# Kernel optimization log

Hardware: AMD Instinct MI355X
Metric: run time of the kernel (lower is better)

## Reference

```python
import jax, jax.numpy as jnp
import numpy as np

B, S, H, NH = 1, 4096, 1024, 16
DH = H // NH


def setup_inputs() -> dict:
    key = jax.random.key(0)
    ks = jax.random.split(key, 9)
    sc = 0.02
    return {
        "queries": jax.random.normal(ks[0], (B, S, H), jnp.float32),
        "keys": jax.random.normal(ks[1], (B, S, H), jnp.float32),
        "values": jax.random.normal(ks[2], (B, S, H), jnp.float32),
        "Wq_w": jax.random.normal(ks[3], (H, H), jnp.float32) * sc,
        "Wq_b": jax.random.normal(ks[4], (H,), jnp.float32) * sc,
        "Wk_w": jax.random.normal(ks[5], (H, H), jnp.float32) * sc,
        "Wk_b": jax.random.normal(ks[6], (H,), jnp.float32) * sc,
        "Wv_w": jax.random.normal(ks[7], (H, H), jnp.float32) * sc,
        "Wv_b": jax.random.normal(ks[8], (H,), jnp.float32) * sc,
    }


def _split_heads(x):
    # torch.chunk(x, NH, dim=-1) then stack(dim=1) == reshape + transpose
    b, s, h = x.shape
    return jnp.transpose(x.reshape(b, s, NH, DH), (0, 2, 1, 3))  # [B,NH,S,DH]


def reference(queries, keys, values, Wq_w, Wq_b, Wk_w, Wk_b, Wv_w, Wv_b):
    q = jax.nn.relu(queries @ Wq_w.T + Wq_b)
    k = jax.nn.relu(keys @ Wk_w.T + Wk_b)
    v = jax.nn.relu(values @ Wv_w.T + Wv_b)
    qh, kh, vh = _split_heads(q), _split_heads(k), _split_heads(v)
    score = jnp.einsum("bhsd,bhtd->bhst", qh, kh) / jnp.sqrt(jnp.float32(DH))
    attn = jax.nn.softmax(score, axis=-1)
    a = jnp.einsum("bhst,bhtd->bhsd", attn, vh)  # [B,NH,S,DH]
    # faithful to torch: permute(0,1,3,2) -> [B,NH,DH,S], then reshape to (B,S,H)
    a = jnp.transpose(a, (0, 1, 3, 2)).reshape(q.shape[0], q.shape[1], q.shape[2])
    return a + queries
```

## Files before the change

kernel.cpp:

```cpp
#include <hip/hip_runtime.h>
#include <stdint.h>


#define SEQ 4096
#define HID 1024
#define NHEAD 16
#define DHEAD 64

typedef __attribute__((ext_vector_type(8))) short short8_t;
typedef __attribute__((ext_vector_type(4))) float f32x4;
typedef __attribute__((ext_vector_type(16))) float f32x16;
typedef __attribute__((ext_vector_type(2))) unsigned int u32x2;

#define WS_QB   0u
#define WS_KB   4194304u
#define WS_VB   8388608u
#define WS_WQ   12582912u
#define WS_QO   15728640u
#define WS_KO   19922944u
#define WS_VT   24117248u

__device__ __forceinline__ unsigned short f2bf(float f) {
  union { float f; unsigned int u; } x; x.f = f;
  unsigned int u = x.u;
  return (unsigned short)((u + 0x7FFFu + ((u >> 16) & 1u)) >> 16);
}

__device__ __forceinline__ float fexp2(float x) {
#if __has_builtin(__builtin_amdgcn_exp2f)
  return __builtin_amdgcn_exp2f(x);
#else
  float r; asm("v_exp_f32 %0, %1" : "=v"(r) : "v"(x)); return r;
#endif
}

__device__ __forceinline__ unsigned int pk2(float a, float b) {
  unsigned int r;
  asm("v_cvt_pk_bf16_f32 %0, %1, %2" : "=v"(r) : "v"(a), "v"(b));
  return r;
}

__device__ __forceinline__ void pl32swap(unsigned int& a, unsigned int& b) {
  asm("v_permlane32_swap_b32 %0, %1" : "+v"(a), "+v"(b));
}

__device__ __forceinline__ void gll16(const void* g, void* l) {
  __builtin_amdgcn_global_load_lds(
      (const __attribute__((address_space(1))) void*)g,
      (__attribute__((address_space(3))) void*)l, 16, 0, 0);
}

__device__ __forceinline__ void packP(const f32x16& a, short8_t& p0,
                                      short8_t& p1) {
  unsigned int w0 = pk2(a[0], a[1]),   w1 = pk2(a[2], a[3]);
  unsigned int w2 = pk2(a[4], a[5]),   w3 = pk2(a[6], a[7]);
  unsigned int w4 = pk2(a[8], a[9]),   w5 = pk2(a[10], a[11]);
  unsigned int w6 = pk2(a[12], a[13]), w7 = pk2(a[14], a[15]);
  pl32swap(w0, w2);
  pl32swap(w1, w3);
  pl32swap(w4, w6);
  pl32swap(w5, w7);
  union { unsigned int u[4]; short8_t v; } q0, q1;
  q0.u[0] = w0; q0.u[1] = w1; q0.u[2] = w2; q0.u[3] = w3;
  q1.u[0] = w4; q1.u[1] = w5; q1.u[2] = w6; q1.u[3] = w7;
  p0 = q0.v; p1 = q1.v;
}

#define MFMA32(a, b, c) __builtin_amdgcn_mfma_f32_32x32x16_bf16(a, b, c, 0, 0, 0)

__global__ void __launch_bounds__(256) prep_convert(
    const float* __restrict__ qin, const float* __restrict__ kin,
    const float* __restrict__ vin, const float* __restrict__ wq,
    const float* __restrict__ wk, const float* __restrict__ wv,
    unsigned short* __restrict__ ws) {
  const int total = 3932160;
  for (int i = blockIdx.x * blockDim.x + threadIdx.x; i < total;
       i += gridDim.x * blockDim.x) {
    const float* src; unsigned short* dst; int off;
    if (i < 3145728) {
      int which = i >> 20;
      off = (i & 1048575) << 2;
      src = which == 0 ? qin : (which == 1 ? kin : vin);
      dst = ws + which * 4194304u;
    } else {
      int j = i - 3145728;
      int which = j >> 18;
      off = (j & 262143) << 2;
      src = which == 0 ? wq : (which == 1 ? wk : wv);
      dst = ws + WS_WQ + which * 1048576u;
    }
    float4 f = *(const float4*)(src + off);
    u32x2 p;
    p.x = f2bf(f.x) | ((unsigned int)f2bf(f.y) << 16);
    p.y = f2bf(f.z) | ((unsigned int)f2bf(f.w) << 16);
    *(u32x2*)(dst + off) = p;
  }
}

__global__ void __launch_bounds__(256) qkv_gemm(
    unsigned short* __restrict__ ws, const float* __restrict__ bq,
    const float* __restrict__ bk, const float* __restrict__ bv) {
  __shared__ alignas(16) unsigned short lA[128 * 64];
  __shared__ alignas(16) unsigned short lB[128 * 64];
  const int z = blockIdx.z;
  const unsigned short* A = ws + z * 4194304u;
  const unsigned short* W = ws + WS_WQ + z * 1048576u;
  const float* bias = z == 0 ? bq : (z == 1 ? bk : bv);
  const int tid = threadIdx.x;
  const int lane = tid & 63;
  const int wid = tid >> 6;
  const int wr = wid >> 1, wc = wid & 1;
  const int lin = blockIdx.y * 8 + blockIdx.x;
  const int nid = (lin & 7) * 32 + (lin >> 3);
  const int bm = nid >> 3, bn = nid & 7;
  const int l15 = lane & 15, l4 = lane >> 4;

  f32x4 acc[4][4];
#pragma unroll
  for (int m = 0; m < 4; ++m)
#pragma unroll
    for (int n = 0; n < 4; ++n) acc[m][n] = {0.f, 0.f, 0.f, 0.f};

  const int srow = tid >> 3;
  const int sch = tid & 7;

  for (int kt = 0; kt < 1024; kt += 64) {
    __syncthreads();
#pragma unroll
    for (int r = 0; r < 4; ++r) {
      const int row = r * 32 + srow;
      const int ch = sch ^ (row & 7);
      gll16(A + (size_t)(bm * 128 + row) * 1024 + kt + ch * 8,
            (char*)lA + r * 4096 + wid * 1024);
      gll16(W + (size_t)(bn * 128 + row) * 1024 + kt + ch * 8,
            (char*)lB + r * 4096 + wid * 1024);
    }
    __syncthreads();
    short8_t af[4][2], bf[4][2];
#pragma unroll
    for (int m = 0; m < 4; ++m) {
      const int row = wr * 64 + m * 16 + l15;
#pragma unroll
      for (int kk = 0; kk < 2; ++kk)
        af[m][kk] = *(const short8_t*)(
            (const char*)lA + row * 128 + (((kk * 4 + l4) ^ (row & 7)) * 16));
    }
#pragma unroll
    for (int n = 0; n < 4; ++n) {
      const int row = wc * 64 + n * 16 + l15;
#pragma unroll
      for (int kk = 0; kk < 2; ++kk)
        bf[n][kk] = *(const short8_t*)(
            (const char*)lB + row * 128 + (((kk * 4 + l4) ^ (row & 7)) * 16));
    }
#pragma unroll
    for (int m = 0; m < 4; ++m)
#pragma unroll
      for (int n = 0; n < 4; ++n)
#pragma unroll
        for (int kk = 0; kk < 2; ++kk)
          acc[m][n] = __builtin_amdgcn_mfma_f32_16x16x32_bf16(
              af[m][kk], bf[n][kk], acc[m][n], 0, 0, 0);
  }

  const int row0 = bm * 128 + wr * 64;
  const int col0 = bn * 128 + wc * 64;
  if (z < 2) {
    const float scl = (z == 1) ? 0.18033688011112042f : 1.0f;
    unsigned short* o = ws + WS_QO + z * 4194304u;
#pragma unroll
    for (int n = 0; n < 4; ++n) {
      const int col = col0 + n * 16 + l15;
      const float bb = bias[col];
#pragma unroll
      for (int m = 0; m < 4; ++m)
#pragma unroll
        for (int j = 0; j < 4; ++j) {
          const int row = row0 + m * 16 + l4 * 4 + j;
          o[(size_t)row * 1024 + col] = f2bf(fmaxf(acc[m][n][j] + bb, 0.f) * scl);
        }
    }
  } else {
    unsigned short* vt = ws + WS_VT;
#pragma unroll
    for (int n = 0; n < 4; ++n) {
      const int col = col0 + n * 16 + l15;
      const float bb = bias[col];
      const int nh = col >> 6, d = col & 63;
#pragma unroll
      for (int m = 0; m < 4; ++m) {
        const int t0 = row0 + m * 16 + l4 * 4;
        u32x2 p;
        p.x = f2bf(fmaxf(acc[m][n][0] + bb, 0.f)) |
              ((unsigned int)f2bf(fmaxf(acc[m][n][1] + bb, 0.f)) << 16);
        p.y = f2bf(fmaxf(acc[m][n][2] + bb, 0.f)) |
              ((unsigned int)f2bf(fmaxf(acc[m][n][3] + bb, 0.f)) << 16);
        *(u32x2*)(vt + (size_t)nh * 262144 + (size_t)d * 4096 + t0) = p;
      }
    }
  }
}

__global__ void __launch_bounds__(512, 4) attn_fwd(
    const unsigned short* __restrict__ ws, const float* __restrict__ qin,
    float* __restrict__ out) {
  __shared__ alignas(16) char smem[32768];
  const char* lKb = smem;
  const char* lVb = smem + 16384;
  float* fO = (float*)smem;
  float* fRs = (float*)(smem + 16896);

  const unsigned short* qo = ws + WS_QO;
  const char* koB = (const char*)(ws + WS_KO);
  const char* vtB = (const char*)(ws + WS_VT);
  const int nh = blockIdx.y;
  const int qb0 = blockIdx.x * 128;
  const int tid = threadIdx.x, lane = tid & 63, wid = tid >> 6;
  const int l31 = lane & 31, l5 = lane >> 5;
  const int qg = wid >> 1, tw = wid & 1;
  const int sq = qb0 + qg * 32 + l31;

  const int stt = tid >> 3;
  const int sch = tid & 7;
  const unsigned kgoff =
      (unsigned)(stt * 1024 + nh * 64 + ((sch ^ (stt & 7)) * 8)) * 2u;
  const unsigned vgoff =
      (unsigned)(nh * 262144 + stt * 4096 + ((sch ^ (stt & 7)) * 8)) * 2u;
  const unsigned ldst = (unsigned)tid * 16u;

  short8_t qf[4];
#pragma unroll
  for (int kcd = 0; kcd < 4; ++kcd)
    qf[kcd] = *(const short8_t*)(qo + (size_t)sq * 1024 + nh * 64 +
                                 kcd * 16 + l5 * 8);

  int kofl[4];
  {
    const int row = tw * 32 + l31;
#pragma unroll
    for (int kcd = 0; kcd < 4; ++kcd)
      kofl[kcd] = row * 128 + (((kcd * 2 + l5) ^ (row & 7)) * 16);
  }
  int vofl[2][2];
#pragma unroll
  for (int n = 0; n < 2; ++n) {
    const int row = n * 32 + l31;
#pragma unroll
    for (int kc = 0; kc < 2; ++kc)
      vofl[n][kc] = row * 128 + (((tw * 4 + kc * 2 + l5) ^ (row & 7)) * 16);
  }

  f32x16 zro;
#pragma unroll
  for (int r = 0; r < 16; ++r) zro[r] = 0.f;
  f32x16 aco0 = zro, aco1 = zro;
  float rs0 = 0.f, rs1 = 0.f, rs2 = 0.f, rs3 = 0.f;

#define STAGE(buf, kvb)                                                        \
  {                                                                            \
    gll16(koB + (kgoff + (unsigned)(kvb) * 2048u),                             \
          (char*)lKb + (buf) * 8192 + ldst);                                   \
    gll16(vtB + (vgoff + (unsigned)(kvb) * 2u),                                \
          (char*)lVb + (buf) * 8192 + ldst);                                   \
  }

  STAGE(0, 0);
  __syncthreads();
  int cur = 0;

  for (int kv = 0; kv < 4096; kv += 64) {
    if (kv + 64 < 4096) STAGE(cur ^ 1, kv + 64);
    const char* lKc = lKb + cur * 8192;
    const char* lVc = lVb + cur * 8192;

    __builtin_amdgcn_s_setprio(1);
    f32x16 acs = MFMA32(*(const short8_t*)(lKc + kofl[0]), qf[0], zro);
#pragma unroll
    for (int kcd = 1; kcd < 4; ++kcd)
      acs = MFMA32(*(const short8_t*)(lKc + kofl[kcd]), qf[kcd], acs);
    __builtin_amdgcn_s_setprio(0);

#pragma unroll
    for (int r = 0; r < 16; r += 4) {
      const float p0 = fexp2(acs[r]);
      const float p1 = fexp2(acs[r + 1]);
      const float p2 = fexp2(acs[r + 2]);
      const float p3 = fexp2(acs[r + 3]);
      acs[r] = p0; acs[r + 1] = p1; acs[r + 2] = p2; acs[r + 3] = p3;
      rs0 += p0; rs1 += p1; rs2 += p2; rs3 += p3;
    }

    short8_t pa0, pa1;
    packP(acs, pa0, pa1);

    const short8_t vf00 = *(const short8_t*)(lVc + vofl[0][0]);
    const short8_t vf10 = *(const short8_t*)(lVc + vofl[1][0]);
    const short8_t vf01 = *(const short8_t*)(lVc + vofl[0][1]);
    const short8_t vf11 = *(const short8_t*)(lVc + vofl[1][1]);
    __builtin_amdgcn_s_setprio(1);
    aco0 = MFMA32(pa0, vf00, aco0);
    aco1 = MFMA32(pa0, vf10, aco1);
    aco0 = MFMA32(pa1, vf01, aco0);
    aco1 = MFMA32(pa1, vf11, aco1);
    __builtin_amdgcn_s_setprio(0);

    __syncthreads();
    cur ^= 1;
  }

  float rs = (rs0 + rs1) + (rs2 + rs3);
  rs += __shfl_xor(rs, 32);

#pragma unroll 1
  for (int p = 0; p < 4; ++p) {
    if (qg == p) {
      float* myO = fO + tw * 2112;
#pragma unroll
      for (int r = 0; r < 16; ++r) {
        const int sl = (r & 3) + 8 * (r >> 2) + 4 * l5;
        myO[l31 * 33 + sl] = aco0[r];
        myO[(l31 + 32) * 33 + sl] = aco1[r];
      }
      if (l5 == 0) fRs[tw * 32 + l31] = rs;
    }
    __syncthreads();
    {
      const int s = tid & 31;
      const int dg = tid >> 5;
      const int sg = qb0 + p * 32 + s;
      const float inv = 1.f / (fRs[s] + fRs[32 + s]);
      const int scol = sg & 1023, srow = sg >> 10;
#pragma unroll
      for (int i = 0; i < 4; ++i) {
        const int d = dg * 4 + i;
        const float v = fO[d * 33 + s] + fO[2112 + d * 33 + s];
        const int idx = (nh * 256 + d * 4 + srow) * 1024 + scol;
        out[idx] = qin[idx] + v * inv;
      }
    }
    __syncthreads();
  }
#undef STAGE
}

extern "C" void kernel_launch(void* const* d_in, const int* in_sizes, int n_in,
                              void* d_out, int out_size, void* d_ws,
                              size_t ws_size, hipStream_t stream) {
  const float* qin = (const float*)d_in[0];
  const float* kin = (const float*)d_in[1];
  const float* vin = (const float*)d_in[2];
  const float* wq = (const float*)d_in[3];
  const float* bq = (const float*)d_in[4];
  const float* wk = (const float*)d_in[5];
  const float* bk = (const float*)d_in[6];
  const float* wv = (const float*)d_in[7];
  const float* bv = (const float*)d_in[8];
  unsigned short* ws = (unsigned short*)d_ws;
  float* out = (float*)d_out;

  prep_convert<<<dim3(8192), dim3(256), 0, stream>>>(qin, kin, vin, wq, wk, wv, ws);
  qkv_gemm<<<dim3(8, 32, 3), dim3(256), 0, stream>>>(ws, bq, bk, bv);
  attn_fwd<<<dim3(32, 16), dim3(512), 0, stream>>>(ws, qin, out);
}
```

Baseline: 134.5 us.

## Fuse fp32-to-bf16 activation conversion into QKV GEMM A-tile loads

The separate pass that converted the q/k/v activations to bf16 in workspace is removed. The QKV GEMM now reads fp32 activations directly into registers, prefetched one k-tile ahead, and packs them to bf16 before writing the swizzled LDS tile. Only the weights are still converted in a smaller prep kernel. This drops the activation round trip through workspace. In exchange each GEMM block reads fp32 A data, which is twice the bytes and is re-read across the 8 N-blocks, and it adds register pressure and VALU packing work inside the main loop.

```diff
diff --git a/kernel.cpp b/kernel.cpp
--- a/kernel.cpp
+++ b/kernel.cpp
@@ -12,9 +12,6 @@
 typedef __attribute__((ext_vector_type(16))) float f32x16;
 typedef __attribute__((ext_vector_type(2))) unsigned int u32x2;
 
-#define WS_QB   0u
-#define WS_KB   4194304u
-#define WS_VB   8388608u
 #define WS_WQ   12582912u
 #define WS_QO   15728640u
 #define WS_KO   19922944u
@@ -68,42 +65,30 @@
 
 #define MFMA32(a, b, c) __builtin_amdgcn_mfma_f32_32x32x16_bf16(a, b, c, 0, 0, 0)
 
-__global__ void __launch_bounds__(256) prep_convert(
-    const float* __restrict__ qin, const float* __restrict__ kin,
-    const float* __restrict__ vin, const float* __restrict__ wq,
-    const float* __restrict__ wk, const float* __restrict__ wv,
-    unsigned short* __restrict__ ws) {
-  const int total = 3932160;
-  for (int i = blockIdx.x * blockDim.x + threadIdx.x; i < total;
-       i += gridDim.x * blockDim.x) {
-    const float* src; unsigned short* dst; int off;
-    if (i < 3145728) {
-      int which = i >> 20;
-      off = (i & 1048575) << 2;
-      src = which == 0 ? qin : (which == 1 ? kin : vin);
-      dst = ws + which * 4194304u;
-    } else {
-      int j = i - 3145728;
-      int which = j >> 18;
-      off = (j & 262143) << 2;
-      src = which == 0 ? wq : (which == 1 ? wk : wv);
-      dst = ws + WS_WQ + which * 1048576u;
-    }
-    float4 f = *(const float4*)(src + off);
-    u32x2 p;
-    p.x = f2bf(f.x) | ((unsigned int)f2bf(f.y) << 16);
-    p.y = f2bf(f.z) | ((unsigned int)f2bf(f.w) << 16);
-    *(u32x2*)(dst + off) = p;
-  }
+__global__ void __launch_bounds__(256) prep_w(
+    const float* __restrict__ wq, const float* __restrict__ wk,
+    const float* __restrict__ wv, unsigned short* __restrict__ ws) {
+  const int i = blockIdx.x * 256 + threadIdx.x;
+  const int which = i >> 18;
+  const int off = (i & 262143) << 2;
+  const float* src = which == 0 ? wq : (which == 1 ? wk : wv);
+  unsigned short* dst = ws + WS_WQ + (unsigned)which * 1048576u;
+  float4 f = *(const float4*)(src + off);
+  u32x2 p;
+  p.x = pk2(f.x, f.y);
+  p.y = pk2(f.z, f.w);
+  *(u32x2*)(dst + off) = p;
 }
 
 __global__ void __launch_bounds__(256) qkv_gemm(
-    unsigned short* __restrict__ ws, const float* __restrict__ bq,
-    const float* __restrict__ bk, const float* __restrict__ bv) {
+    unsigned short* __restrict__ ws, const float* __restrict__ qin,
+    const float* __restrict__ kin, const float* __restrict__ vin,
+    const float* __restrict__ bq, const float* __restrict__ bk,
+    const float* __restrict__ bv) {
   __shared__ alignas(16) unsigned short lA[128 * 64];
   __shared__ alignas(16) unsigned short lB[128 * 64];
   const int z = blockIdx.z;
-  const unsigned short* A = ws + z * 4194304u;
+  const float* A32 = z == 0 ? qin : (z == 1 ? kin : vin);
   const unsigned short* W = ws + WS_WQ + z * 1048576u;
   const float* bias = z == 0 ? bq : (z == 1 ? bk : bv);
   const int tid = threadIdx.x;
@@ -124,18 +109,43 @@
   const int srow = tid >> 3;
   const int sch = tid & 7;
 
+  float4 ar[4][2];
+#define LOADA(kt_)                                                             \
+  {                                                                            \
+    _Pragma("unroll") for (int rr = 0; rr < 4; ++rr) {                         \
+      const int row = rr * 32 + srow;                                          \
+      const float* s_ = A32 + (size_t)(bm * 128 + row) * 1024 + (kt_) +        \
+                        sch * 8;                                               \
+      ar[rr][0] = *(const float4*)(s_);                                        \
+      ar[rr][1] = *(const float4*)(s_ + 4);                                    \
+    }                                                                          \
+  }
+#define WRITEA()                                                               \
+  {                                                                            \
+    _Pragma("unroll") for (int rr = 0; rr < 4; ++rr) {                         \
+      const int row = rr * 32 + srow;                                          \
+      union { unsigned int u[4]; short8_t v; } t_;                             \
+      t_.u[0] = pk2(ar[rr][0].x, ar[rr][0].y);                                 \
+      t_.u[1] = pk2(ar[rr][0].z, ar[rr][0].w);                                 \
+      t_.u[2] = pk2(ar[rr][1].x, ar[rr][1].y);                                 \
+      t_.u[3] = pk2(ar[rr][1].z, ar[rr][1].w);                                 \
+      *(short8_t*)((char*)lA + row * 128 + (((sch ^ (row & 7))) * 16)) = t_.v; \
+    }                                                                          \
+  }
+
+  LOADA(0);
   for (int kt = 0; kt < 1024; kt += 64) {
     __syncthreads();
+    WRITEA();
 #pragma unroll
     for (int r = 0; r < 4; ++r) {
       const int row = r * 32 + srow;
       const int ch = sch ^ (row & 7);
-      gll16(A + (size_t)(bm * 128 + row) * 1024 + kt + ch * 8,
-            (char*)lA + r * 4096 + wid * 1024);
       gll16(W + (size_t)(bn * 128 + row) * 1024 + kt + ch * 8,
             (char*)lB + r * 4096 + wid * 1024);
     }
     __syncthreads();
+    if (kt + 64 < 1024) LOADA(kt + 64);
     short8_t af[4][2], bf[4][2];
 #pragma unroll
     for (int m = 0; m < 4; ++m) {
@@ -162,6 +172,8 @@
           acc[m][n] = __builtin_amdgcn_mfma_f32_16x16x32_bf16(
               af[m][kk], bf[n][kk], acc[m][n], 0, 0, 0);
   }
+#undef LOADA
+#undef WRITEA
 
   const int row0 = bm * 128 + wr * 64;
   const int col0 = bn * 128 + wc * 64;
@@ -358,7 +370,8 @@
   unsigned short* ws = (unsigned short*)d_ws;
   float* out = (float*)d_out;
 
-  prep_convert<<<dim3(8192), dim3(256), 0, stream>>>(qin, kin, vin, wq, wk, wv, ws);
-  qkv_gemm<<<dim3(8, 32, 3), dim3(256), 0, stream>>>(ws, bq, bk, bv);
+  prep_w<<<dim3(3072), dim3(256), 0, stream>>>(wq, wk, wv, ws);
+  qkv_gemm<<<dim3(8, 32, 3), dim3(256), 0, stream>>>(ws, qin, kin, vin,
+                                                     bq, bk, bv);
   attn_fwd<<<dim3(32, 16), dim3(512), 0, stream>>>(ws, qin, out);
 }
```

Result: faster. 130.9 us (median of 2 runs) (-2.7%).
